# Kernel tuning notes

Hardware: AMD Instinct MI355X
Metric: run time of the kernel (lower is better)

The kernel has to match this reference:

```python
import jax, jax.numpy as jnp
import numpy as np

B, Z, H, T = 256, 512, 2048, 16
EPS = 1e-5

def _normalize(v):
    return v / (jnp.linalg.norm(v) + 1e-12)

def setup_inputs() -> dict:
    key = jax.random.key(0)
    ks = jax.random.split(key, 10)
    s = lambda fan: 1.0 / np.sqrt(fan)
    return {
        "z": jax.random.normal(ks[0], (B, Z), dtype=jnp.float32),
        "fc_w": jax.random.normal(ks[1], (Z, Z), dtype=jnp.float32) * s(Z),
        "fc_b": jnp.zeros((Z,), dtype=jnp.float32),
        "fc_u": _normalize(jax.random.normal(ks[2], (Z,), dtype=jnp.float32)),
        "w_ih": jax.random.normal(ks[3], (3 * H, Z), dtype=jnp.float32) * s(Z),
        "w_hh": jax.random.normal(ks[4], (3 * H, H), dtype=jnp.float32) * s(H),
        "b_ih": jnp.zeros((3 * H,), dtype=jnp.float32).at[H:2 * H].set(1.0),  # forget-gate bias init
        "b_hh": jnp.zeros((3 * H,), dtype=jnp.float32),
        "lin_w": jax.random.normal(ks[5], (Z, H), dtype=jnp.float32) * s(H),
        "lin_b": jnp.zeros((Z,), dtype=jnp.float32),
    }

def _spectral_norm(w, u):
    # one torch-style power iteration (u, v treated as constants)
    v = jax.lax.stop_gradient(_normalize(w.T @ u))
    u1 = jax.lax.stop_gradient(_normalize(w @ v))
    sigma = u1 @ (w @ v)
    return w / sigma

def reference(z, fc_w, fc_b, fc_u, w_ih, w_hh, b_ih, b_hh, lin_w, lin_b):
    # spectral-norm linear: h0 = z @ (W/sigma)^T + b
    w_sn = _spectral_norm(fc_w, fc_u)
    x0 = z @ w_sn.T + fc_b                      # [B, Z]
    h0 = jnp.zeros((B, H), dtype=z.dtype)       # initHidden

    def step(carry, _):
        x, h = carry
        gi = x @ w_ih.T + b_ih                  # [B, 3H]
        gh = h @ w_hh.T + b_hh                  # [B, 3H]
        i_r, i_z, i_n = jnp.split(gi, 3, axis=1)
        h_r, h_z, h_n = jnp.split(gh, 3, axis=1)
        r = jax.nn.sigmoid(i_r + h_r)
        u = jax.nn.sigmoid(i_z + h_z)
        n = jnp.tanh(i_n + r * h_n)
        h_new = (1.0 - u) * n + u * h
        x_new = h_new @ lin_w.T + lin_b         # [B, Z] fed back as next input
        return (x_new, h_new), x_new

    _, outs = jax.lax.scan(step, (x0, h0), None, length=T)  # [T, B, Z]

    # per-timestep BatchNorm1d(affine=False), training-mode batch stats
    mean = jnp.mean(outs, axis=1, keepdims=True)
    var = jnp.mean((outs - mean) ** 2, axis=1, keepdims=True)
    y = (outs - mean) / jnp.sqrt(var + EPS)     # [T, B, Z]

    y = jnp.transpose(y, (1, 0, 2))             # [B, T, Z]
    return y.reshape(-1, Z)                     # [B*T, Z]
```

## Files before the change

kernel.cpp:

```cpp
#include <hip/hip_runtime.h>
#include <hip/hip_bf16.h>
#include <cstdint>
#include <cstddef>

#define B_  256
#define Z_  512
#define H_  2048
#define T_  16
#define H3_ 6144

using short8  = __attribute__((ext_vector_type(8))) short;
using bf16x8  = __attribute__((ext_vector_type(8))) __bf16;
using f32x4   = __attribute__((ext_vector_type(4))) float;
using f32x16  = __attribute__((ext_vector_type(16))) float;

__device__ __forceinline__ f32x4 mfma_bf16(short8 a, short8 b, f32x4 c) {
  return __builtin_amdgcn_mfma_f32_16x16x32_bf16(
      __builtin_bit_cast(bf16x8, a), __builtin_bit_cast(bf16x8, b), c, 0, 0, 0);
}
__device__ __forceinline__ f32x16 mfma_bf16_32(short8 a, short8 b, f32x16 c) {
  return __builtin_amdgcn_mfma_f32_32x32x16_bf16(
      __builtin_bit_cast(bf16x8, a), __builtin_bit_cast(bf16x8, b), c, 0, 0, 0);
}

__device__ __forceinline__ unsigned short f2bf(float f) {
  unsigned int u = __builtin_bit_cast(unsigned int, f);
  u = (u + 0x7FFFu + ((u >> 16) & 1u)) >> 16;
  return (unsigned short)u;
}

__device__ __forceinline__ float sigmoidf_(float x) { return 1.0f / (1.0f + __expf(-x)); }

__device__ __forceinline__ int swz(int row, int chunk) {
  return row * 64 + ((chunk ^ (row & 7)) << 3);
}

__global__ __launch_bounds__(512, 1) void gru_step4(
    const unsigned short* __restrict__ A, int K,
    const unsigned short* __restrict__ Wr,
    const unsigned short* __restrict__ Wz,
    const unsigned short* __restrict__ Wn,
    const unsigned short* __restrict__ Whn,
    const float* __restrict__ cr, const float* __restrict__ cz,
    const float* __restrict__ cn, const float* __restrict__ chn,
    float hn_scale,
    const float* __restrict__ h_old,
    float* __restrict__ h_new,
    unsigned short* __restrict__ h_hist)
{
  __shared__ __align__(16) unsigned short sbuf[2][12288];
  __shared__ float LDSf[4][64][33];
  const int bid = blockIdx.x, tid = threadIdx.x;
  const int xcd = bid & 7, rst = bid >> 3;
  const int m_idx = rst & 3, gg = rst >> 2;
  const int grp = gg * 8 + xcd;
  const int m0 = m_idx * 64;
  const int gh0 = grp * 32;
  const int wave = tid >> 6, lane = tid & 63;
  const int gate = wave & 3, mh = wave >> 2;
  const int lh = lane >> 5, l31 = lane & 31;

  const int arow = tid >> 3, achk = tid & 7;
  const int wrow = tid >> 2, wc0 = (tid & 3) * 2;
  const unsigned short* wsrc =
      (wrow < 32) ? Wr : (wrow < 64) ? Wz : (wrow < 96) ? Wn : Whn;
  const size_t aoff = (size_t)(m0 + arow) * K + achk * 8;
  const size_t woff = (size_t)(gh0 + (wrow & 31)) * K + wc0 * 8;
  const int sa_d  = swz(arow, achk);
  const int sw_d0 = 4096 + swz(wrow, wc0 + 0);
  const int sw_d1 = 4096 + swz(wrow, wc0 + 1);

  uint4 Aa, Aw0, Aw1;
  uint4 Ba, Bw0, Bw1;

#define LDSET(a, w0, w1, k0)                               \
  {                                                        \
    const int kk_ = (k0);                                  \
    a  = *(const uint4*)(A    + aoff + kk_);               \
    w0 = *(const uint4*)(wsrc + woff + kk_);               \
    w1 = *(const uint4*)(wsrc + woff + kk_ + 8);           \
  }
#define STAGE(s, a, w0, w1)                                \
  {                                                        \
    unsigned short* b_ = sbuf[s];                          \
    *(uint4*)(b_ + sa_d)  = a;                             \
    *(uint4*)(b_ + sw_d0) = w0;                            \
    *(uint4*)(b_ + sw_d1) = w1;                            \
  }

  f32x16 acc = {};
#define COMP(s)                                                            \
  {                                                                        \
    const unsigned short* b_ = sbuf[s];                                    \
    _Pragma("unroll")                                                      \
    for (int ks = 0; ks < 4; ++ks) {                                       \
      short8 af = *(const short8*)(b_ + swz(mh * 32 + l31, ks * 2 + lh));  \
      short8 wf = *(const short8*)(b_ + 4096 + swz(gate * 32 + l31, ks * 2 + lh)); \
      acc = mfma_bf16_32(af, wf, acc);                                     \
    }                                                                      \
  }

  const int nIter = K >> 6;
  LDSET(Aa, Aw0, Aw1, 0);
  LDSET(Ba, Bw0, Bw1, 64);
  for (int it = 0; it < nIter; it += 2) {
    STAGE(0, Aa, Aw0, Aw1);
    __syncthreads();
    { const int kn = (it + 2 < nIter) ? ((it + 2) << 6) : 0;
      LDSET(Aa, Aw0, Aw1, kn); }
    COMP(0);
    STAGE(1, Ba, Bw0, Bw1);
    __syncthreads();
    { const int kn = (it + 3 < nIter) ? ((it + 3) << 6) : 64;
      LDSET(Ba, Bw0, Bw1, kn); }
    COMP(1);
  }
#undef LDSET
#undef STAGE
#undef COMP

#pragma unroll
  for (int reg = 0; reg < 16; ++reg) {
    const int trow = (reg & 3) + 8 * (reg >> 2) + 4 * lh;
    LDSf[gate][mh * 32 + trow][l31] = acc[reg];
  }
  __syncthreads();
  {
    const int row = tid >> 3, c0 = (tid & 7) * 4;
    const int grow = m0 + row;
#pragma unroll
    for (int j = 0; j < 4; ++j) {
      const int col = c0 + j;
      const int gcol = gh0 + col;
      const float R   = sigmoidf_(LDSf[0][row][col] + cr[gcol]);
      const float U   = sigmoidf_(LDSf[1][row][col] + cz[gcol]);
      const float HNv = hn_scale * LDSf[3][row][col] + chn[gcol];
      const float Nv  = tanhf(LDSf[2][row][col] + cn[gcol] + R * HNv);
      const float ho  = h_old ? h_old[(size_t)grow * H_ + gcol] : 0.0f;
      const float hv  = (1.0f - U) * Nv + U * ho;
      h_new[(size_t)grow * H_ + gcol]  = hv;
      h_hist[(size_t)grow * H_ + gcol] = f2bf(hv);
    }
  }
}

__global__ __launch_bounds__(256) void gemm_bt(
    const unsigned short* __restrict__ A,
    const unsigned short* __restrict__ Bw,
    int K,
    const float* __restrict__ addsrc, int add_ld,
    const float* __restrict__ bias,
    const float* __restrict__ scale_ptr,
    unsigned short* __restrict__ out_bf,
    float* __restrict__ out_f, int ldo)
{
  __shared__ unsigned short sA[32 * 64];
  __shared__ unsigned short sB[64 * 64];
  const int tid  = threadIdx.x;
  const int m0   = blockIdx.x * 32, n0 = blockIdx.y * 64;
  const int wave = tid >> 6, lane = tid & 63;
  const int wr = wave & 1, wc = wave >> 1;
  const int q = lane >> 4, c16 = lane & 15;
  const int lr = tid >> 3, lc8 = tid & 7;
  f32x4 acc0 = {}, acc1 = {};
  const size_t rowA  = (size_t)(m0 + lr) * K;
  const size_t rowB0 = (size_t)(n0 + lr) * K;
  const size_t rowB1 = (size_t)(n0 + 32 + lr) * K;
  for (int k0 = 0; k0 < K; k0 += 64) {
    const int gc = k0 + lc8 * 8;
    uint4 ra  = *(const uint4*)(A  + rowA  + gc);
    uint4 rb0 = *(const uint4*)(Bw + rowB0 + gc);
    uint4 rb1 = *(const uint4*)(Bw + rowB1 + gc);
    __syncthreads();
    *(uint4*)(sA + swz(lr, lc8))      = ra;
    *(uint4*)(sB + swz(lr, lc8))      = rb0;
    *(uint4*)(sB + swz(32 + lr, lc8)) = rb1;
    __syncthreads();
#pragma unroll
    for (int kk = 0; kk < 2; ++kk) {
      const int arow = wr * 16 + c16;
      short8 af = *(const short8*)(sA + swz(arow, kk * 4 + q));
      const int brow = wc * 32 + c16;
      short8 b0 = *(const short8*)(sB + swz(brow, kk * 4 + q));
      acc0 = mfma_bf16(af, b0, acc0);
      short8 b1 = *(const short8*)(sB + swz(brow + 16, kk * 4 + q));
      acc1 = mfma_bf16(af, b1, acc1);
    }
  }
  const float scale = scale_ptr ? *scale_ptr : 1.0f;
#pragma unroll
  for (int cf = 0; cf < 2; ++cf) {
    f32x4 a = cf ? acc1 : acc0;
#pragma unroll
    for (int v = 0; v < 4; ++v) {
      const int row = m0 + wr * 16 + q * 4 + v;
      const int col = n0 + wc * 32 + cf * 16 + c16;
      float val = a[v] * scale;
      if (addsrc) val += addsrc[(size_t)row * add_ld + col];
      if (bias)   val += bias[col];
      if (out_f)  out_f[(size_t)row * ldo + col] = val;
      if (out_bf) out_bf[(size_t)row * ldo + col] = f2bf(val);
    }
  }
}

__global__ __launch_bounds__(256) void gemm_bt64(
    const unsigned short* __restrict__ A,
    const unsigned short* __restrict__ Bw,
    int K,
    const float* __restrict__ addsrc, int add_ld,
    const float* __restrict__ bias,
    unsigned short* __restrict__ out_bf,
    float* __restrict__ out_f, int ldo)
{
  __shared__ unsigned short sA[64 * 64];
  __shared__ unsigned short sB[64 * 64];
  const int tid  = threadIdx.x;
  const int m0   = blockIdx.x * 64, n0 = blockIdx.y * 64;
  const int wave = tid >> 6, lane = tid & 63;
  const int wr = wave & 1, wc = wave >> 1;
  const int q = lane >> 4, c16 = lane & 15;
  const int lr = tid >> 3, lc8 = tid & 7;
  f32x4 acc[2][2] = {};
  const size_t aoff = (size_t)(m0 + lr) * K;
  const size_t boff = (size_t)(n0 + lr) * K;
  const size_t s32  = (size_t)32 * K;

  uint4 ra0, ra1, rb0, rb1;
  auto LOAD = [&](int k0) {
    const int gc = k0 + lc8 * 8;
    ra0 = *(const uint4*)(A  + aoff + gc);
    ra1 = *(const uint4*)(A  + aoff + s32 + gc);
    rb0 = *(const uint4*)(Bw + boff + gc);
    rb1 = *(const uint4*)(Bw + boff + s32 + gc);
  };

  const int nIter = K >> 6;
  LOAD(0);
  for (int it = 0; it < nIter; ++it) {
    __syncthreads();
    *(uint4*)(sA + swz(lr, lc8))      = ra0;
    *(uint4*)(sA + swz(lr + 32, lc8)) = ra1;
    *(uint4*)(sB + swz(lr, lc8))      = rb0;
    *(uint4*)(sB + swz(lr + 32, lc8)) = rb1;
    __syncthreads();
    if (it + 1 < nIter) LOAD((it + 1) << 6);
#pragma unroll
    for (int kk = 0; kk < 2; ++kk) {
      short8 af0 = *(const short8*)(sA + swz(wr * 32 + c16,      kk * 4 + q));
      short8 af1 = *(const short8*)(sA + swz(wr * 32 + 16 + c16, kk * 4 + q));
      short8 bf0 = *(const short8*)(sB + swz(wc * 32 + c16,      kk * 4 + q));
      short8 bf1 = *(const short8*)(sB + swz(wc * 32 + 16 + c16, kk * 4 + q));
      acc[0][0] = mfma_bf16(af0, bf0, acc[0][0]);
      acc[0][1] = mfma_bf16(af0, bf1, acc[0][1]);
      acc[1][0] = mfma_bf16(af1, bf0, acc[1][0]);
      acc[1][1] = mfma_bf16(af1, bf1, acc[1][1]);
    }
  }
#pragma unroll
  for (int i = 0; i < 2; ++i) {
#pragma unroll
    for (int j = 0; j < 2; ++j) {
#pragma unroll
      for (int v = 0; v < 4; ++v) {
        const int row = m0 + wr * 32 + i * 16 + q * 4 + v;
        const int col = n0 + wc * 32 + j * 16 + c16;
        float val = acc[i][j][v];
        if (addsrc) val += addsrc[(size_t)row * add_ld + col];
        if (bias)   val += bias[col];
        if (out_f)  out_f[(size_t)row * ldo + col] = val;
        if (out_bf) out_bf[(size_t)row * ldo + col] = f2bf(val);
      }
    }
  }
}

__global__ __launch_bounds__(256) void quant_all(
    const float* __restrict__ z, const float* __restrict__ fc_w,
    const float* __restrict__ w_ih, const float* __restrict__ w_hh,
    const float* __restrict__ lin_w,
    unsigned short* __restrict__ z_q, unsigned short* __restrict__ fc_w_q,
    unsigned short* __restrict__ w_ih_q, unsigned short* __restrict__ w_hhn_q,
    unsigned short* __restrict__ lin_w_q)
{
  const int i = blockIdx.x * 256 + threadIdx.x;
  if (i >= 2195456) return;
  const float4* src; ushort4* dst; int idx;
  if (i < 32768)        { src = (const float4*)z;     dst = (ushort4*)z_q;     idx = i; }
  else if (i < 98304)   { src = (const float4*)fc_w;  dst = (ushort4*)fc_w_q;  idx = i - 32768; }
  else if (i < 884736)  { src = (const float4*)w_ih;  dst = (ushort4*)w_ih_q;  idx = i - 98304; }
  else if (i < 1933312) { src = (const float4*)(w_hh + (size_t)2 * H_ * H_);
                          dst = (ushort4*)w_hhn_q;    idx = i - 884736; }
  else                  { src = (const float4*)lin_w; dst = (ushort4*)lin_w_q; idx = i - 1933312; }
  float4 v = src[idx];
  ushort4 o; o.x = f2bf(v.x); o.y = f2bf(v.y); o.z = f2bf(v.z); o.w = f2bf(v.w);
  dst[idx] = o;
}

__global__ __launch_bounds__(256) void transq(const float* __restrict__ s,
                                              unsigned short* __restrict__ d) {
  __shared__ float tile[32][33];
  const int tx = threadIdx.x & 31, ty = threadIdx.x >> 5;
  const int k0 = blockIdx.x * 32, z0 = blockIdx.y * 32;
#pragma unroll
  for (int j = 0; j < 4; ++j)
    tile[ty + j * 8][tx] = s[(size_t)(z0 + ty + j * 8) * H_ + k0 + tx];
  __syncthreads();
#pragma unroll
  for (int j = 0; j < 4; ++j)
    d[(size_t)(k0 + ty + j * 8) * Z_ + z0 + tx] = f2bf(tile[tx][ty + j * 8]);
}

__global__ void sigma1(const float* __restrict__ W, const float* __restrict__ u,
                       float* __restrict__ t1) {
  __shared__ float part[4][64];
  const int lane = threadIdx.x & 63, wv = threadIdx.x >> 6;
  const int col = blockIdx.x * 64 + lane;
  float s = 0.f;
  for (int r = wv * 128; r < wv * 128 + 128; ++r)
    s += W[(size_t)r * Z_ + col] * u[r];
  part[wv][lane] = s;
  __syncthreads();
  if (wv == 0)
    t1[col] = part[0][lane] + part[1][lane] + part[2][lane] + part[3][lane];
}

__global__ void sigma1b(const float* __restrict__ t1, float* __restrict__ invn) {
  __shared__ float red[256];
  int t = threadIdx.x;
  float v0 = t1[t], v1 = t1[t + 256];
  red[t] = v0 * v0 + v1 * v1;
  __syncthreads();
  for (int s = 128; s > 0; s >>= 1) {
    if (t < s) red[t] += red[t + s];
    __syncthreads();
  }
  if (t == 0) invn[0] = 1.0f / (sqrtf(red[0]) + 1e-12f);
}

__global__ void sigma2(const float* __restrict__ W, const float* __restrict__ t1,
                       const float* __restrict__ invn, float* __restrict__ t2) {
  const int lane = threadIdx.x & 63, wv = threadIdx.x >> 6;
  const int row = blockIdx.x * 4 + wv;
  float s = 0.f;
  for (int c = lane; c < Z_; c += 64) s += W[(size_t)row * Z_ + c] * t1[c];
#pragma unroll
  for (int off = 32; off > 0; off >>= 1) s += __shfl_down(s, off);
  if (lane == 0) t2[row] = s * invn[0];
}

__global__ void sigma3(const float* __restrict__ t2, float* __restrict__ inv_sig) {
  __shared__ float red[256];
  int t = threadIdx.x;
  float v0 = t2[t], v1 = t2[t + 256];
  red[t] = v0 * v0 + v1 * v1;
  __syncthreads();
  for (int s = 128; s > 0; s >>= 1) {
    if (t < s) red[t] += red[t + s];
    __syncthreads();
  }
  if (t == 0) {
    float s2  = red[0];
    float sig = s2 / (sqrtf(s2) + 1e-12f);
    inv_sig[0] = 1.0f / sig;
  }
}

__global__ __launch_bounds__(256) void dots_k(const float* __restrict__ w,
                                              const float* __restrict__ lb,
                                              float* __restrict__ dvec) {
  const int wave = threadIdx.x >> 6, lane = threadIdx.x & 63;
#pragma unroll
  for (int i = 0; i < 4; ++i) {
    int row = blockIdx.x * 16 + wave * 4 + i;
    float s = 0.f;
    for (int c = lane; c < Z_; c += 64) s += w[(size_t)row * Z_ + c] * lb[c];
#pragma unroll
    for (int off = 32; off > 0; off >>= 1) s += __shfl_down(s, off);
    if (lane == 0) dvec[row] = s;
  }
}

__global__ void consts_k(const float* __restrict__ b_ih, const float* __restrict__ b_hh,
                         const float* __restrict__ dvec,
                         float* __restrict__ c0r, float* __restrict__ c0z,
                         float* __restrict__ c0n,
                         float* __restrict__ c1r, float* __restrict__ c1z,
                         float* __restrict__ c1n, float* __restrict__ chn) {
  int j = blockIdx.x * 256 + threadIdx.x;
  float br = b_ih[j], bz = b_ih[H_ + j], bn = b_ih[2 * H_ + j];
  float hr = b_hh[j], hz = b_hh[H_ + j], hn = b_hh[2 * H_ + j];
  c0r[j] = br + hr; c0z[j] = bz + hz; c0n[j] = bn; chn[j] = hn;
  c1r[j] = br + hr + dvec[j];
  c1z[j] = bz + hz + dvec[H_ + j];
  c1n[j] = bn + dvec[2 * H_ + j];
}

__global__ __launch_bounds__(256) void bn_k(const float* __restrict__ outs,
                                            float* __restrict__ y) {
  __shared__ float s_sum[4][64], s_sq[4][64], s_mean[64], s_inv[64];
  const int t = blockIdx.x, zb = blockIdx.y;
  const int zl = threadIdx.x & 63, bp = threadIdx.x >> 6;
  const int z = zb * 64 + zl;
  float sum = 0.f, sq = 0.f;
  for (int b = bp * 64; b < bp * 64 + 64; ++b) {
    float v = outs[(size_t)(t * 256 + b) * Z_ + z];
    sum += v; sq += v * v;
  }
  s_sum[bp][zl] = sum; s_sq[bp][zl] = sq;
  __syncthreads();
  if (bp == 0) {
    float S = s_sum[0][zl] + s_sum[1][zl] + s_sum[2][zl] + s_sum[3][zl];
    float Q = s_sq[0][zl] + s_sq[1][zl] + s_sq[2][zl] + s_sq[3][zl];
    float mean = S * (1.0f / 256.0f);
    float var  = Q * (1.0f / 256.0f) - mean * mean;
    s_mean[zl] = mean;
    s_inv[zl]  = rsqrtf(var + 1e-5f);
  }
  __syncthreads();
  const float mean = s_mean[zl], inv = s_inv[zl];
  for (int b = bp * 64; b < bp * 64 + 64; ++b) {
    float v = outs[(size_t)(t * 256 + b) * Z_ + z];
    y[(size_t)(b * T_ + t) * Z_ + z] = (v - mean) * inv;
  }
}

extern "C" void kernel_launch(void* const* d_in, const int* in_sizes, int n_in,
                              void* d_out, int out_size, void* d_ws, size_t ws_size,
                              hipStream_t stream) {
  const float* z     = (const float*)d_in[0];
  const float* fc_w  = (const float*)d_in[1];
  const float* fc_b  = (const float*)d_in[2];
  const float* fc_u  = (const float*)d_in[3];
  const float* w_ih  = (const float*)d_in[4];
  const float* w_hh  = (const float*)d_in[5];
  const float* b_ih  = (const float*)d_in[6];
  const float* b_hh  = (const float*)d_in[7];
  const float* lin_w = (const float*)d_in[8];
  const float* lin_b = (const float*)d_in[9];
  float* out = (float*)d_out;

  char* ws = (char*)d_ws;
  size_t off = 0;
  auto alloc = [&](size_t bytes) -> void* {
    off = (off + 255) & ~(size_t)255;
    void* p = ws + off;
    off += bytes;
    return p;
  };
  unsigned short* w_ih_q   = (unsigned short*)alloc((size_t)H3_ * Z_ * 2);
  unsigned short* w_hhn_q  = (unsigned short*)alloc((size_t)H_ * H_ * 2);
  unsigned short* lin_w_q  = (unsigned short*)alloc((size_t)Z_ * H_ * 2);
  unsigned short* lin_wT_q = (unsigned short*)alloc((size_t)Z_ * H_ * 2);
  unsigned short* fc_w_q   = (unsigned short*)alloc((size_t)Z_ * Z_ * 2);
  unsigned short* z_q      = (unsigned short*)alloc((size_t)B_ * Z_ * 2);
  unsigned short* x0_q     = (unsigned short*)alloc((size_t)B_ * Z_ * 2);
  unsigned short* Wsum_r   = (unsigned short*)alloc((size_t)H_ * H_ * 2);
  unsigned short* Wsum_z   = (unsigned short*)alloc((size_t)H_ * H_ * 2);
  unsigned short* Wn_c     = (unsigned short*)alloc((size_t)H_ * H_ * 2);
  unsigned short* Hhist    = (unsigned short*)alloc((size_t)T_ * B_ * H_ * 2);
  float* h_f32 = (float*)alloc((size_t)2 * B_ * H_ * 4);
  float* outs  = (float*)alloc((size_t)T_ * B_ * Z_ * 4);
  float* c0r = (float*)alloc(H_ * 4);
  float* c0z = (float*)alloc(H_ * 4);
  float* c0n = (float*)alloc(H_ * 4);
  float* c1r = (float*)alloc(H_ * 4);
  float* c1z = (float*)alloc(H_ * 4);
  float* c1n = (float*)alloc(H_ * 4);
  float* chn = (float*)alloc(H_ * 4);
  float* dvec = (float*)alloc(H3_ * 4);
  float* t1v = (float*)alloc(Z_ * 4);
  float* t2v = (float*)alloc(Z_ * 4);
  float* invn = (float*)alloc(256);
  float* invsig = (float*)alloc(256);
  (void)in_sizes; (void)n_in; (void)out_size; (void)ws_size;

  quant_all<<<dim3((2195456 + 255) / 256), 256, 0, stream>>>(
      z, fc_w, w_ih, w_hh, lin_w, z_q, fc_w_q, w_ih_q, w_hhn_q, lin_w_q);
  transq<<<dim3(64, 16), 256, 0, stream>>>(lin_w, lin_wT_q);
  sigma1<<<8, 256, 0, stream>>>(fc_w, fc_u, t1v);
  sigma1b<<<1, 256, 0, stream>>>(t1v, invn);
  sigma2<<<128, 256, 0, stream>>>(fc_w, t1v, invn, t2v);
  sigma3<<<1, 256, 0, stream>>>(t2v, invsig);
  dots_k<<<384, 256, 0, stream>>>(w_ih, lin_b, dvec);
  consts_k<<<8, 256, 0, stream>>>(b_ih, b_hh, dvec, c0r, c0z, c0n, c1r, c1z, c1n, chn);

  gemm_bt<<<dim3(B_ / 32, Z_ / 64), 256, 0, stream>>>(
      z_q, fc_w_q, Z_, nullptr, 0, fc_b, invsig, x0_q, nullptr, Z_);

  for (int g = 0; g < 3; ++g) {
    const float* adds = (g < 2) ? (w_hh + (size_t)g * H_ * H_) : nullptr;
    unsigned short* outw = (g == 0) ? Wsum_r : (g == 1) ? Wsum_z : Wn_c;
    gemm_bt64<<<dim3(H_ / 64, H_ / 64), 256, 0, stream>>>(
        w_ih_q + (size_t)g * H_ * Z_, lin_wT_q, Z_, adds, H_, nullptr,
        outw, nullptr, H_);
  }

  for (int t = 0; t < T_; ++t) {
    if (t == 0) {
      gru_step4<<<256, 512, 0, stream>>>(
          x0_q, Z_,
          w_ih_q, w_ih_q + (size_t)H_ * Z_, w_ih_q + (size_t)2 * H_ * Z_,
          w_ih_q ,
          c0r, c0z, c0n, chn, 0.0f, nullptr, h_f32, Hhist);
    } else {
      gru_step4<<<256, 512, 0, stream>>>(
          Hhist + (size_t)(t - 1) * B_ * H_, H_,
          Wsum_r, Wsum_z, Wn_c, w_hhn_q,
          c1r, c1z, c1n, chn, 1.0f,
          h_f32 + (size_t)((t - 1) & 1) * B_ * H_,
          h_f32 + (size_t)(t & 1) * B_ * H_,
          Hhist + (size_t)t * B_ * H_);
    }
  }

  gemm_bt64<<<dim3(T_ * B_ / 64, Z_ / 64), 256, 0, stream>>>(
      Hhist, lin_w_q, H_, nullptr, 0, lin_b, nullptr, outs, Z_);

  bn_k<<<dim3(T_, Z_ / 64), 256, 0, stream>>>(outs, out);
}
```

Before: 402.9 us.

## Restructure GRU step to 256 threads with 2x2 register tiles and split-K reduction

The GRU step kernel drops from 8 waves to 4. Each wave now computes a 2x2 block of 32x32 MFMA tiles over half the K chunk of every stage, and the two K-halves are summed through shared memory before the gate epilogue. Fragments loaded from shared memory are reused across two tiles, which cuts LDS read traffic per MFMA, at the cost of fewer waves to hide latency and an extra reduction pass. Separately, the three weight-sum GEMM launches are merged into one grid, and several small setup kernels (sigma1b/sigma2, dots_k/consts_k) are fused to cut launch count.

```diff
diff --git a/kernel.cpp b/kernel.cpp
--- a/kernel.cpp
+++ b/kernel.cpp
@@ -35,7 +35,7 @@
   return row * 64 + ((chunk ^ (row & 7)) << 3);
 }
 
-__global__ __launch_bounds__(512, 1) void gru_step4(
+__global__ __launch_bounds__(256, 1) void gru_step5(
     const unsigned short* __restrict__ A, int K,
     const unsigned short* __restrict__ Wr,
     const unsigned short* __restrict__ Wz,
@@ -57,79 +57,124 @@
   const int m0 = m_idx * 64;
   const int gh0 = grp * 32;
   const int wave = tid >> 6, lane = tid & 63;
-  const int gate = wave & 3, mh = wave >> 2;
+  const int kk = wave & 1, gp = wave >> 1;
   const int lh = lane >> 5, l31 = lane & 31;
 
-  const int arow = tid >> 3, achk = tid & 7;
-  const int wrow = tid >> 2, wc0 = (tid & 3) * 2;
+  const int arow = tid >> 2, ac0 = (tid & 3) * 2;
+  const int wrow = tid >> 1, wc0 = (tid & 1) * 4;
   const unsigned short* wsrc =
-      (wrow < 32) ? Wr : (wrow < 64) ? Wz : (wrow < 96) ? Wn : Whn;
-  const size_t aoff = (size_t)(m0 + arow) * K + achk * 8;
+      (wave == 0) ? Wr : (wave == 1) ? Wz : (wave == 2) ? Wn : Whn;
+  const size_t aoff = (size_t)(m0 + arow) * K + ac0 * 8;
   const size_t woff = (size_t)(gh0 + (wrow & 31)) * K + wc0 * 8;
-  const int sa_d  = swz(arow, achk);
+  const int sa_d0 = swz(arow, ac0);
+  const int sa_d1 = swz(arow, ac0 + 1);
   const int sw_d0 = 4096 + swz(wrow, wc0 + 0);
   const int sw_d1 = 4096 + swz(wrow, wc0 + 1);
-
-  uint4 Aa, Aw0, Aw1;
-  uint4 Ba, Bw0, Bw1;
-
-#define LDSET(a, w0, w1, k0)                               \
+  const int sw_d2 = 4096 + swz(wrow, wc0 + 2);
+  const int sw_d3 = 4096 + swz(wrow, wc0 + 3);
+
+  uint4 Aa0, Aa1, Aw0, Aw1, Aw2, Aw3;
+  uint4 Ba0, Ba1, Bw0, Bw1, Bw2, Bw3;
+
+#define LDSET(a0, a1, w0, w1, w2, w3, k0)                  \
   {                                                        \
     const int kk_ = (k0);                                  \
-    a  = *(const uint4*)(A    + aoff + kk_);               \
+    a0 = *(const uint4*)(A    + aoff + kk_);               \
+    a1 = *(const uint4*)(A    + aoff + kk_ + 8);           \
     w0 = *(const uint4*)(wsrc + woff + kk_);               \
     w1 = *(const uint4*)(wsrc + woff + kk_ + 8);           \
-  }
-#define STAGE(s, a, w0, w1)                                \
+    w2 = *(const uint4*)(wsrc + woff + kk_ + 16);          \
+    w3 = *(const uint4*)(wsrc + woff + kk_ + 24);          \
+  }
+#define STAGE(s, a0, a1, w0, w1, w2, w3)                   \
   {                                                        \
     unsigned short* b_ = sbuf[s];                          \
-    *(uint4*)(b_ + sa_d)  = a;                             \
+    *(uint4*)(b_ + sa_d0) = a0;                            \
+    *(uint4*)(b_ + sa_d1) = a1;                            \
     *(uint4*)(b_ + sw_d0) = w0;                            \
     *(uint4*)(b_ + sw_d1) = w1;                            \
-  }
-
-  f32x16 acc = {};
+    *(uint4*)(b_ + sw_d2) = w2;                            \
+    *(uint4*)(b_ + sw_d3) = w3;                            \
+  }
+
+  f32x16 acc00 = {}, acc01 = {}, acc10 = {}, acc11 = {};
+  const int g0r = (gp * 2) * 32, g1r = (gp * 2 + 1) * 32;
+
 #define COMP(s)                                                            \
   {                                                                        \
     const unsigned short* b_ = sbuf[s];                                    \
     _Pragma("unroll")                                                      \
-    for (int ks = 0; ks < 4; ++ks) {                                       \
-      short8 af = *(const short8*)(b_ + swz(mh * 32 + l31, ks * 2 + lh));  \
-      short8 wf = *(const short8*)(b_ + 4096 + swz(gate * 32 + l31, ks * 2 + lh)); \
-      acc = mfma_bf16_32(af, wf, acc);                                     \
+    for (int ksi = 0; ksi < 2; ++ksi) {                                    \
+      const int ch = kk * 4 + ksi * 2 + lh;                                \
+      short8 af0 = *(const short8*)(b_ + swz(l31, ch));                    \
+      short8 af1 = *(const short8*)(b_ + swz(32 + l31, ch));               \
+      short8 wf0 = *(const short8*)(b_ + 4096 + swz(g0r + l31, ch));       \
+      short8 wf1 = *(const short8*)(b_ + 4096 + swz(g1r + l31, ch));       \
+      acc00 = mfma_bf16_32(af0, wf0, acc00);                               \
+      acc01 = mfma_bf16_32(af0, wf1, acc01);                               \
+      acc10 = mfma_bf16_32(af1, wf0, acc10);                               \
+      acc11 = mfma_bf16_32(af1, wf1, acc11);                               \
     }                                                                      \
   }
 
   const int nIter = K >> 6;
-  LDSET(Aa, Aw0, Aw1, 0);
-  LDSET(Ba, Bw0, Bw1, 64);
+  LDSET(Aa0, Aa1, Aw0, Aw1, Aw2, Aw3, 0);
+  LDSET(Ba0, Ba1, Bw0, Bw1, Bw2, Bw3, 64);
   for (int it = 0; it < nIter; it += 2) {
-    STAGE(0, Aa, Aw0, Aw1);
+    STAGE(0, Aa0, Aa1, Aw0, Aw1, Aw2, Aw3);
     __syncthreads();
     { const int kn = (it + 2 < nIter) ? ((it + 2) << 6) : 0;
-      LDSET(Aa, Aw0, Aw1, kn); }
+      LDSET(Aa0, Aa1, Aw0, Aw1, Aw2, Aw3, kn); }
     COMP(0);
-    STAGE(1, Ba, Bw0, Bw1);
+    STAGE(1, Ba0, Ba1, Bw0, Bw1, Bw2, Bw3);
     __syncthreads();
     { const int kn = (it + 3 < nIter) ? ((it + 3) << 6) : 64;
-      LDSET(Ba, Bw0, Bw1, kn); }
+      LDSET(Ba0, Ba1, Bw0, Bw1, Bw2, Bw3, kn); }
     COMP(1);
   }
 #undef LDSET
 #undef STAGE
 #undef COMP
 
-#pragma unroll
-  for (int reg = 0; reg < 16; ++reg) {
-    const int trow = (reg & 3) + 8 * (reg >> 2) + 4 * lh;
-    LDSf[gate][mh * 32 + trow][l31] = acc[reg];
-  }
+  __syncthreads();
+  float* red = (float*)sbuf;
+#define RSLOT(t, r) ((((gp << 2) | (t)) * 16 + (r)) * 64 + lane)
+  if (kk == 1) {
+#pragma unroll
+    for (int r = 0; r < 16; ++r) red[RSLOT(0, r)] = acc00[r];
+#pragma unroll
+    for (int r = 0; r < 16; ++r) red[RSLOT(1, r)] = acc01[r];
+#pragma unroll
+    for (int r = 0; r < 16; ++r) red[RSLOT(2, r)] = acc10[r];
+#pragma unroll
+    for (int r = 0; r < 16; ++r) red[RSLOT(3, r)] = acc11[r];
+  }
+  __syncthreads();
+  if (kk == 0) {
+#pragma unroll
+    for (int r = 0; r < 16; ++r) acc00[r] += red[RSLOT(0, r)];
+#pragma unroll
+    for (int r = 0; r < 16; ++r) acc01[r] += red[RSLOT(1, r)];
+#pragma unroll
+    for (int r = 0; r < 16; ++r) acc10[r] += red[RSLOT(2, r)];
+#pragma unroll
+    for (int r = 0; r < 16; ++r) acc11[r] += red[RSLOT(3, r)];
+#pragma unroll
+    for (int r = 0; r < 16; ++r) {
+      const int trow = (r & 3) + 8 * (r >> 2) + 4 * lh;
+      LDSf[gp * 2    ][trow     ][l31] = acc00[r];
+      LDSf[gp * 2 + 1][trow     ][l31] = acc01[r];
+      LDSf[gp * 2    ][32 + trow][l31] = acc10[r];
+      LDSf[gp * 2 + 1][32 + trow][l31] = acc11[r];
+    }
+  }
+#undef RSLOT
   __syncthreads();
   {
-    const int row = tid >> 3, c0 = (tid & 7) * 4;
+    const int row = tid >> 2, c0 = (tid & 3) * 8;
     const int grow = m0 + row;
 #pragma unroll
-    for (int j = 0; j < 4; ++j) {
+    for (int j = 0; j < 8; ++j) {
       const int col = c0 + j;
       const int gcol = gh0 + col;
       const float R   = sigmoidf_(LDSf[0][row][col] + cr[gcol]);
@@ -204,19 +249,18 @@
   }
 }
 
-__global__ __launch_bounds__(256) void gemm_bt64(
+__device__ __forceinline__ void dev_gemm64core(
+    unsigned short* sA, unsigned short* sB,
     const unsigned short* __restrict__ A,
     const unsigned short* __restrict__ Bw,
     int K,
     const float* __restrict__ addsrc, int add_ld,
     const float* __restrict__ bias,
     unsigned short* __restrict__ out_bf,
-    float* __restrict__ out_f, int ldo)
-{
-  __shared__ unsigned short sA[64 * 64];
-  __shared__ unsigned short sB[64 * 64];
+    float* __restrict__ out_f, int ldo, int mi, int ni)
+{
   const int tid  = threadIdx.x;
-  const int m0   = blockIdx.x * 64, n0 = blockIdx.y * 64;
+  const int m0   = mi * 64, n0 = ni * 64;
   const int wave = tid >> 6, lane = tid & 63;
   const int wr = wave & 1, wc = wave >> 1;
   const int q = lane >> 4, c16 = lane & 15;
@@ -273,6 +317,38 @@
       }
     }
   }
+}
+
+__global__ __launch_bounds__(256) void gemm_bt64(
+    const unsigned short* __restrict__ A,
+    const unsigned short* __restrict__ Bw,
+    int K,
+    const float* __restrict__ addsrc, int add_ld,
+    const float* __restrict__ bias,
+    unsigned short* __restrict__ out_bf,
+    float* __restrict__ out_f, int ldo)
+{
+  __shared__ unsigned short sA[64 * 64];
+  __shared__ unsigned short sB[64 * 64];
+  dev_gemm64core(sA, sB, A, Bw, K, addsrc, add_ld, bias, out_bf, out_f, ldo,
+                 blockIdx.x, blockIdx.y);
+}
+
+__global__ __launch_bounds__(256) void gemm_wsum(
+    const unsigned short* __restrict__ w_ih_q,
+    const unsigned short* __restrict__ lin_wT_q,
+    const float* __restrict__ w_hh,
+    unsigned short* __restrict__ Wsum_r,
+    unsigned short* __restrict__ Wsum_z,
+    unsigned short* __restrict__ Wn_c)
+{
+  __shared__ unsigned short sA[64 * 64];
+  __shared__ unsigned short sB[64 * 64];
+  const int g = blockIdx.y >> 5, ni = blockIdx.y & 31;
+  const float* adds = (g < 2) ? (w_hh + (size_t)g * H_ * H_) : nullptr;
+  unsigned short* outw = (g == 0) ? Wsum_r : (g == 1) ? Wsum_z : Wn_c;
+  dev_gemm64core(sA, sB, w_ih_q + (size_t)g * H_ * Z_, lin_wT_q, Z_,
+                 adds, H_, nullptr, outw, nullptr, H_, blockIdx.x, ni);
 }
 
 __global__ __launch_bounds__(256) void quant_all(
@@ -325,28 +401,26 @@
     t1[col] = part[0][lane] + part[1][lane] + part[2][lane] + part[3][lane];
 }
 
-__global__ void sigma1b(const float* __restrict__ t1, float* __restrict__ invn) {
+__global__ void sigma2(const float* __restrict__ W, const float* __restrict__ t1,
+                       float* __restrict__ t2) {
   __shared__ float red[256];
-  int t = threadIdx.x;
-  float v0 = t1[t], v1 = t1[t + 256];
-  red[t] = v0 * v0 + v1 * v1;
+  const int tid = threadIdx.x;
+  float p = 0.f;
+  for (int c = tid; c < Z_; c += 256) { float v = t1[c]; p += v * v; }
+  red[tid] = p;
   __syncthreads();
   for (int s = 128; s > 0; s >>= 1) {
-    if (t < s) red[t] += red[t + s];
-    __syncthreads();
-  }
-  if (t == 0) invn[0] = 1.0f / (sqrtf(red[0]) + 1e-12f);
-}
-
-__global__ void sigma2(const float* __restrict__ W, const float* __restrict__ t1,
-                       const float* __restrict__ invn, float* __restrict__ t2) {
-  const int lane = threadIdx.x & 63, wv = threadIdx.x >> 6;
+    if (tid < s) red[tid] += red[tid + s];
+    __syncthreads();
+  }
+  const float invn = 1.0f / (sqrtf(red[0]) + 1e-12f);
+  const int lane = tid & 63, wv = tid >> 6;
   const int row = blockIdx.x * 4 + wv;
   float s = 0.f;
   for (int c = lane; c < Z_; c += 64) s += W[(size_t)row * Z_ + c] * t1[c];
 #pragma unroll
   for (int off = 32; off > 0; off >>= 1) s += __shfl_down(s, off);
-  if (lane == 0) t2[row] = s * invn[0];
+  if (lane == 0) t2[row] = s * invn;
 }
 
 __global__ void sigma3(const float* __restrict__ t2, float* __restrict__ inv_sig) {
@@ -366,9 +440,13 @@
   }
 }
 
-__global__ __launch_bounds__(256) void dots_k(const float* __restrict__ w,
-                                              const float* __restrict__ lb,
-                                              float* __restrict__ dvec) {
+__global__ __launch_bounds__(256) void dots2_k(
+    const float* __restrict__ w, const float* __restrict__ lb,
+    const float* __restrict__ b_ih, const float* __restrict__ b_hh,
+    float* __restrict__ c0r, float* __restrict__ c0z, float* __restrict__ c0n,
+    float* __restrict__ c1r, float* __restrict__ c1z, float* __restrict__ c1n,
+    float* __restrict__ chn)
+{
   const int wave = threadIdx.x >> 6, lane = threadIdx.x & 63;
 #pragma unroll
   for (int i = 0; i < 4; ++i) {
@@ -377,23 +455,14 @@
     for (int c = lane; c < Z_; c += 64) s += w[(size_t)row * Z_ + c] * lb[c];
 #pragma unroll
     for (int off = 32; off > 0; off >>= 1) s += __shfl_down(s, off);
-    if (lane == 0) dvec[row] = s;
-  }
-}
-
-__global__ void consts_k(const float* __restrict__ b_ih, const float* __restrict__ b_hh,
-                         const float* __restrict__ dvec,
-                         float* __restrict__ c0r, float* __restrict__ c0z,
-                         float* __restrict__ c0n,
-                         float* __restrict__ c1r, float* __restrict__ c1z,
-                         float* __restrict__ c1n, float* __restrict__ chn) {
-  int j = blockIdx.x * 256 + threadIdx.x;
-  float br = b_ih[j], bz = b_ih[H_ + j], bn = b_ih[2 * H_ + j];
-  float hr = b_hh[j], hz = b_hh[H_ + j], hn = b_hh[2 * H_ + j];
-  c0r[j] = br + hr; c0z[j] = bz + hz; c0n[j] = bn; chn[j] = hn;
-  c1r[j] = br + hr + dvec[j];
-  c1z[j] = bz + hz + dvec[H_ + j];
-  c1n[j] = bn + dvec[2 * H_ + j];
+    if (lane == 0) {
+      const int g = row >> 11, j = row & 2047;
+      const float bi = b_ih[row], bh = b_hh[row];
+      if (g == 0)      { c0r[j] = bi + bh; c1r[j] = bi + bh + s; }
+      else if (g == 1) { c0z[j] = bi + bh; c1z[j] = bi + bh + s; }
+      else             { c0n[j] = bi;      c1n[j] = bi + s;      chn[j] = bh; }
+    }
+  }
 }
 
 __global__ __launch_bounds__(256) void bn_k(const float* __restrict__ outs,
@@ -468,10 +537,8 @@
   float* c1z = (float*)alloc(H_ * 4);
   float* c1n = (float*)alloc(H_ * 4);
   float* chn = (float*)alloc(H_ * 4);
-  float* dvec = (float*)alloc(H3_ * 4);
   float* t1v = (float*)alloc(Z_ * 4);
   float* t2v = (float*)alloc(Z_ * 4);
-  float* invn = (float*)alloc(256);
   float* invsig = (float*)alloc(256);
   (void)in_sizes; (void)n_in; (void)out_size; (void)ws_size;
 
@@ -479,32 +546,26 @@
       z, fc_w, w_ih, w_hh, lin_w, z_q, fc_w_q, w_ih_q, w_hhn_q, lin_w_q);
   transq<<<dim3(64, 16), 256, 0, stream>>>(lin_w, lin_wT_q);
   sigma1<<<8, 256, 0, stream>>>(fc_w, fc_u, t1v);
-  sigma1b<<<1, 256, 0, stream>>>(t1v, invn);
-  sigma2<<<128, 256, 0, stream>>>(fc_w, t1v, invn, t2v);
+  sigma2<<<128, 256, 0, stream>>>(fc_w, t1v, t2v);
   sigma3<<<1, 256, 0, stream>>>(t2v, invsig);
-  dots_k<<<384, 256, 0, stream>>>(w_ih, lin_b, dvec);
-  consts_k<<<8, 256, 0, stream>>>(b_ih, b_hh, dvec, c0r, c0z, c0n, c1r, c1z, c1n, chn);
+  dots2_k<<<384, 256, 0, stream>>>(w_ih, lin_b, b_ih, b_hh,
+                                   c0r, c0z, c0n, c1r, c1z, c1n, chn);
 
   gemm_bt<<<dim3(B_ / 32, Z_ / 64), 256, 0, stream>>>(
       z_q, fc_w_q, Z_, nullptr, 0, fc_b, invsig, x0_q, nullptr, Z_);
 
-  for (int g = 0; g < 3; ++g) {
-    const float* adds = (g < 2) ? (w_hh + (size_t)g * H_ * H_) : nullptr;
-    unsigned short* outw = (g == 0) ? Wsum_r : (g == 1) ? Wsum_z : Wn_c;
-    gemm_bt64<<<dim3(H_ / 64, H_ / 64), 256, 0, stream>>>(
-        w_ih_q + (size_t)g * H_ * Z_, lin_wT_q, Z_, adds, H_, nullptr,
-        outw, nullptr, H_);
-  }
+  gemm_wsum<<<dim3(H_ / 64, 96), 256, 0, stream>>>(
+      w_ih_q, lin_wT_q, w_hh, Wsum_r, Wsum_z, Wn_c);
 
   for (int t = 0; t < T_; ++t) {
     if (t == 0) {
-      gru_step4<<<256, 512, 0, stream>>>(
+      gru_step5<<<256, 256, 0, stream>>>(
           x0_q, Z_,
           w_ih_q, w_ih_q + (size_t)H_ * Z_, w_ih_q + (size_t)2 * H_ * Z_,
           w_ih_q ,
           c0r, c0z, c0n, chn, 0.0f, nullptr, h_f32, Hhist);
     } else {
-      gru_step4<<<256, 512, 0, stream>>>(
+      gru_step5<<<256, 256, 0, stream>>>(
           Hhist + (size_t)(t - 1) * B_ * H_, H_,
           Wsum_r, Wsum_z, Wn_c, w_hhn_q,
           c1r, c1z, c1n, chn, 1.0f,
```

Measured after the change: 446.3 us. 10.8% more time.
